# Optimization experiments

Measured on AMD Instinct MI355X. Metric: run time of the kernel, lower is better.

## Reference

```python
import jax, jax.numpy as jnp
import numpy as np

L, B, S, D, N, H = 4, 4, 1024, 1024, 64, 16   # layers, batch, seq, d_model, d_state, heads
DI = 2 * D      # d_inner (expand_factor=2)
DH = D // H     # head dim
DF = 4 * D      # ffn hidden
SCALE = 1.0 / np.sqrt(DH)


def setup_inputs() -> dict:
    key = jax.random.key(0)
    ks = jax.random.split(key, 12)
    w = lambda k, sh: jax.random.normal(k, sh, jnp.float32) * 0.02
    return {
        "x": jax.random.normal(ks[0], (B, S, D), jnp.float32),
        "A_log": jax.random.normal(ks[1], (L, N), jnp.float32),
        "Dp": jax.random.normal(ks[2], (L, D), jnp.float32),
        "W_in": w(ks[3], (L, 2 * DI, D)), "b_in": jnp.zeros((L, 2 * DI), jnp.float32),
        "W_xp": w(ks[4], (L, N, DI)), "b_xp": jnp.zeros((L, N), jnp.float32),
        "W_dt": w(ks[5], (L, D, DI)), "b_dt": jnp.zeros((L, D), jnp.float32),
        "W_out": w(ks[6], (L, D, DI)), "b_out": jnp.zeros((L, D), jnp.float32),
        "W_qkv": w(ks[7], (L, 3 * D, D)), "b_qkv": jnp.zeros((L, 3 * D), jnp.float32),
        "W_ao": w(ks[8], (L, D, D)), "b_ao": jnp.zeros((L, D), jnp.float32),
        "g1": jnp.ones((L, D), jnp.float32), "be1": jnp.zeros((L, D), jnp.float32),
        "g2": jnp.ones((L, D), jnp.float32), "be2": jnp.zeros((L, D), jnp.float32),
        "W_f1": w(ks[9], (L, DF, D)), "b_f1": jnp.zeros((L, DF), jnp.float32),
        "W_f2": w(ks[10], (L, D, DF)), "b_f2": jnp.zeros((L, D), jnp.float32),
    }


def _ln(x, g, b, eps=1e-5):
    mu = x.mean(-1, keepdims=True)
    var = ((x - mu) ** 2).mean(-1, keepdims=True)
    return (x - mu) * jax.lax.rsqrt(var + eps) * g + b


def _mamba(x, A_log, Dp, W_in, b_in, W_xp, b_xp, W_dt, b_dt, W_out, b_out):
    xr = jnp.einsum('bsd,od->bso', x, W_in) + b_in          # [b,s,2*DI]
    xi, res = jnp.split(xr, 2, axis=-1)
    xi = jax.nn.silu(xi)
    A = -jnp.exp(A_log)                                      # [N]
    delta = jax.nn.softplus(jnp.einsum('bsi,di->bsd', xi, W_dt) + b_dt)  # [b,s,D]
    m = delta.mean(-1)                                       # [b,s]
    A_disc = jnp.exp(A[None, None, :] * m[:, :, None])       # [b,s,N]
    u = jnp.einsum('bsi,ni->bsn', xi, W_xp) + b_xp           # [b,s,N]

    def step(state, inp):
        a_t, u_t = inp
        state = a_t * state + u_t                            # [b,N]
        return state, state.sum(-1)                          # carry, emit sum over d_state

    init = jnp.zeros((x.shape[0], A_log.shape[0]), x.dtype)
    _, ssum = jax.lax.scan(step, init, (A_disc.swapaxes(0, 1), u.swapaxes(0, 1)))
    ssum = ssum.swapaxes(0, 1)                               # [b,s]
    y = ssum[..., None] * xi                                 # [b,s,DI]
    y = y * jax.nn.silu(res)
    y = jnp.einsum('bsi,di->bsd', y, W_out) + b_out
    return y + x * Dp


def _attn(x, W_qkv, b_qkv, W_ao, b_ao):
    b, s, d = x.shape
    qkv = jnp.einsum('bsd,od->bso', x, W_qkv) + b_qkv        # [b,s,3d]
    qkv = qkv.reshape(b, s, 3, H, DH)
    q = jnp.moveaxis(qkv[:, :, 0], 2, 1)                     # [b,h,s,dh]
    k = jnp.moveaxis(qkv[:, :, 1], 2, 1)
    v = jnp.moveaxis(qkv[:, :, 2], 2, 1)
    scores = jnp.einsum('bhqd,bhkd->bhqk', q, k) * SCALE
    wts = jax.nn.softmax(scores, axis=-1)
    o = jnp.einsum('bhqk,bhkd->bhqd', wts, v)
    o = jnp.moveaxis(o, 1, 2).reshape(b, s, d)
    return jnp.einsum('bsd,od->bso', o, W_ao) + b_ao


def _forward(x, A_log, Dp, W_in, b_in, W_xp, b_xp, W_dt, b_dt, W_out, b_out,
             W_qkv, b_qkv, W_ao, b_ao, g1, be1, g2, be2, W_f1, b_f1, W_f2, b_f2):
    for l in range(L):
        m = _mamba(x, A_log[l], Dp[l], W_in[l], b_in[l], W_xp[l], b_xp[l],
                   W_dt[l], b_dt[l], W_out[l], b_out[l])
        x = _ln(x + m, g1[l], be1[l])
        a = _attn(x, W_qkv[l], b_qkv[l], W_ao[l], b_ao[l])
        x = _ln(x + a, g2[l], be2[l])
        h = jax.nn.gelu(jnp.einsum('bsd,fd->bsf', x, W_f1[l]) + b_f1[l], approximate=False)
        x = x + jnp.einsum('bsf,df->bsd', h, W_f2[l]) + b_f2[l]
    return x


def reference(x, A_log, Dp, W_in, b_in, W_xp, b_xp, W_dt, b_dt, W_out, b_out,
              W_qkv, b_qkv, W_ao, b_ao, g1, be1, g2, be2, W_f1, b_f1, W_f2, b_f2):
    return _forward(x, A_log, Dp, W_in, b_in, W_xp, b_xp, W_dt, b_dt, W_out, b_out,
                    W_qkv, b_qkv, W_ao, b_ao, g1, be1, g2, be2, W_f1, b_f1, W_f2, b_f2)
```

## Files before the change

kernel.cpp:

```cpp
#include <hip/hip_runtime.h>
#include <math.h>

typedef unsigned short ushort_t;
typedef unsigned int uint_t;
typedef __attribute__((ext_vector_type(8))) short short8;
typedef __attribute__((ext_vector_type(4))) float f32x4;

constexpr int Bb = 4, Ss = 1024, Dd = 1024, Nn = 64, Hh = 16;
constexpr int DIi = 2048, DFf = 4096;
constexpr int TOKENS = Bb * Ss;

constexpr size_t O_IN  = 0;
constexpr size_t O_DT  = 4194304;
constexpr size_t O_XP  = O_DT + 2097152;
constexpr size_t O_OUT = O_XP + 262144;
constexpr size_t O_QKV = O_OUT + 2097152;
constexpr size_t O_AO  = O_QKV + 3145728;
constexpr size_t O_F1  = O_AO + 1048576;
constexpr size_t O_F2  = O_F1 + 4194304;
constexpr size_t W_TOTAL = O_F2 + 4194304;
constexpr size_t W_QUADS = W_TOTAL / 4;

enum { EPI_SPLIT = 0, EPI_QKV, EPI_GELU, EPI_DTXP, EPI_DP, EPI_F32, EPI_RESID };

__device__ __forceinline__ float siluf(float x) { return x / (1.f + expf(-x)); }
__device__ __forceinline__ float softplusf(float x) { return fmaxf(x, 0.f) + log1pf(expf(-fabsf(x))); }
__device__ __forceinline__ float geluf(float x) { return 0.5f * x * (1.f + erff(x * 0.7071067811865476f)); }

__device__ __forceinline__ float bf2f(uint_t u) {
    union { uint_t i; float f; } v; v.i = u << 16; return v.f;
}
__device__ __forceinline__ ushort_t f2bf(float f) {
    union { float f; uint_t i; } v; v.f = f;
    return (ushort_t)((v.i + 0x7FFFu + ((v.i >> 16) & 1u)) >> 16);
}

__device__ __forceinline__ void gload_lds16(const ushort_t* g, ushort_t* l) {
    __builtin_amdgcn_global_load_lds(
        (const __attribute__((address_space(1))) unsigned int*)g,
        (__attribute__((address_space(3))) unsigned int*)l, 16, 0, 0);
}

__device__ __forceinline__ void wait_vm(int n) {
    if (n == 0)      asm volatile("s_waitcnt vmcnt(0)" ::: "memory");
    else if (n == 3) asm volatile("s_waitcnt vmcnt(3)" ::: "memory");
    else if (n == 4) asm volatile("s_waitcnt vmcnt(4)" ::: "memory");
    else if (n == 6) asm volatile("s_waitcnt vmcnt(6)" ::: "memory");
    else             asm volatile("s_waitcnt vmcnt(8)" ::: "memory");
}

template <int EPI>
__global__ __launch_bounds__(512, 2) void gemm_wide256(
    const ushort_t* __restrict__ A, const ushort_t* __restrict__ Bw,
    const float* __restrict__ bias, int M, int N, int K,
    ushort_t* __restrict__ ob0, ushort_t* __restrict__ ob1)
{
    __shared__ __attribute__((aligned(16))) ushort_t AB[65536];
    const int tid = threadIdx.x;
    const int lane = tid & 63, wid = tid >> 6;
    const int wr = wid >> 2, wc = wid & 3;
    const int l15 = lane & 15, lg = lane >> 4;

    int bx = blockIdx.x, by = blockIdx.y;
    const int gx = gridDim.x, gy = gridDim.y;
    if ((gy & 3) == 0 && (gx & 1) == 0) {
        const int s = by * gx + bx;
        const int xcd = s & 7, c = s >> 3;
        const int gyc = gy >> 2, gxc = gx >> 1;
        by = (xcd & 3) * gyc + (c % gyc);
        bx = (xcd >> 2) * gxc + (c / gyc);
    }
    const int m0 = by << 8, n0 = bx << 8;

    f32x4 acc[8][4];
#pragma unroll
    for (int i = 0; i < 8; ++i)
#pragma unroll
        for (int j = 0; j < 4; ++j) { acc[i][j][0]=0.f; acc[i][j][1]=0.f; acc[i][j][2]=0.f; acc[i][j][3]=0.f; }

    const int srow8 = lane >> 3;
    const int scc8  = (lane & 7) ^ srow8;
    const ushort_t* Ag = A + (size_t)(m0 + wid * 32 + srow8) * K + scc8 * 8;
    const ushort_t* Bg = Bw + (size_t)(n0 + wid * 32 + srow8) * K + scc8 * 8;

    auto STAGE = [&](int b_, int k0_) {
        ushort_t* d_ = AB + b_ * 32768;
#pragma unroll
        for (int i = 0; i < 4; ++i) {
            gload_lds16(Ag + (size_t)i * 8 * K + k0_, d_ + (wid * 32 + i * 8) * 64);
            gload_lds16(Bg + (size_t)i * 8 * K + k0_, d_ + 16384 + (wid * 32 + i * 8) * 64);
        }
    };

    const int NS = K >> 6;
    STAGE(0, 0);
    wait_vm(0);
    __builtin_amdgcn_s_barrier();
    int cur = 0;
    for (int s = 0; s < NS; ++s) {
        if (s + 1 < NS) STAGE(cur ^ 1, (s + 1) << 6);
        const ushort_t* As_ = AB + cur * 32768;
        const ushort_t* Bs_ = As_ + 16384;
#pragma unroll
        for (int kk = 0; kk < 2; ++kk) {
            short8 af[8], bfr[4];
#pragma unroll
            for (int mi = 0; mi < 8; ++mi) {
                const int row = wr * 128 + mi * 16 + l15;
                const int ch = (kk * 4 + lg) ^ (row & 7);
                af[mi] = *(const short8*)&As_[row * 64 + ch * 8];
            }
#pragma unroll
            for (int nj = 0; nj < 4; ++nj) {
                const int row = wc * 64 + nj * 16 + l15;
                const int ch = (kk * 4 + lg) ^ (row & 7);
                bfr[nj] = *(const short8*)&Bs_[row * 64 + ch * 8];
            }
#pragma unroll
            for (int mi = 0; mi < 8; ++mi)
#pragma unroll
                for (int nj = 0; nj < 4; ++nj)
                    acc[mi][nj] = __builtin_amdgcn_mfma_f32_16x16x32_bf16(
                        af[mi], bfr[nj], acc[mi][nj], 0, 0, 0);
        }
        if (s + 1 < NS) {
            wait_vm(0);
            __builtin_amdgcn_s_barrier();
        }
        cur ^= 1;
    }
    __syncthreads();

    const bool lo = (EPI != EPI_SPLIT) || (n0 < DIi);
#pragma unroll
    for (int nj = 0; nj < 4; ++nj) {
        const int coll = wc * 64 + nj * 16 + l15;
        const float bv = bias[n0 + coll];
#pragma unroll
        for (int mi = 0; mi < 8; ++mi)
#pragma unroll
            for (int r = 0; r < 4; ++r) {
                float v = acc[mi][nj][r] + bv;
                if (EPI == EPI_SPLIT) v = lo ? siluf(v) : v;
                else v = geluf(v);
                AB[(wr * 128 + mi * 16 + lg * 4 + r) * 256 + coll] = f2bf(v);
            }
    }
    __syncthreads();
    ushort_t* dst = (EPI == EPI_SPLIT) ? (lo ? ob0 : ob1) : ob0;
    const int Nd = (EPI == EPI_SPLIT) ? DIi : N;
    const int nb = (EPI == EPI_SPLIT && !lo) ? (n0 - DIi) : n0;
#pragma unroll
    for (int it = 0; it < 16; ++it) {
        const int c = it * 512 + tid;
        const int row = c >> 5, ch = c & 31;
        *(uint4*)&dst[(size_t)(m0 + row) * Nd + nb + ch * 8] =
            *(const uint4*)&AB[row * 256 + ch * 8];
    }
}

template <int EPI, int MT, int NBUF, int XBY>
__global__ __launch_bounds__(256) void gemm_mfma(
    const ushort_t* __restrict__ A, const ushort_t* __restrict__ Bw,
    const float* __restrict__ bias, int M, int N, int K,
    float* __restrict__ of0, float* __restrict__ of1,
    ushort_t* __restrict__ ob0, ushort_t* __restrict__ ob1,
    const float* __restrict__ e0, const float* __restrict__ e1)
{
    constexpr int BUFSZ = (MT == 128) ? 8192 : 6144;
    constexpr int DEPTH = NBUF - 1;
    constexpr int L     = (MT == 128) ? 4 : 3;
    constexpr int NJ    = (MT == 128) ? 4 : 2;
    constexpr int XBX   = 8 / XBY;
    __shared__ __attribute__((aligned(16))) ushort_t AB[NBUF * BUFSZ];

    const int tid = threadIdx.x;
    const int lane = tid & 63, wid = tid >> 6;
    const int wr = (MT == 128) ? (wid >> 1) : 0;
    const int wc = (MT == 128) ? (wid & 1) : wid;
    const int l15 = lane & 15, lg = lane >> 4;

    int bx = blockIdx.x, by = blockIdx.y;
    const int gx = gridDim.x, gy = gridDim.y;
    if ((gy % XBY) == 0 && (gx % XBX) == 0) {
        const int s = by * gx + bx;
        const int xcd = s & 7, c = s >> 3;
        const int gyc = gy / XBY, gxc = gx / XBX;
        by = (xcd % XBY) * gyc + (c % gyc);
        bx = (xcd / XBY) * gxc + (c / gyc);
    }
    const int m0 = by * MT, n0 = bx << 7;

    f32x4 acc[4][NJ];
#pragma unroll
    for (int i = 0; i < 4; ++i)
#pragma unroll
        for (int j = 0; j < NJ; ++j) { acc[i][j][0] = 0.f; acc[i][j][1] = 0.f; acc[i][j][2] = 0.f; acc[i][j][3] = 0.f; }

    const int srow4 = lane >> 2;
    const int scc4  = (lane & 3) ^ ((lane >> 3) & 3);
    const ushort_t* Ag = A + (size_t)(m0 + wid * 32 + srow4) * K + scc4 * 8;
    const ushort_t* Bg = Bw + (size_t)(n0 + wid * 32 + srow4) * K + scc4 * 8;
    const ushort_t* sb64[3];
    int do64[3];
    if (MT == 64) {
#pragma unroll
        for (int j = 0; j < 3; ++j) {
            const int i = wid * 3 + j;
            const bool isA = i < 4;
            const int rb = (isA ? i : i - 4) * 16;
            sb64[j] = (isA ? A + (size_t)(m0 + rb + srow4) * K
                           : Bw + (size_t)(n0 + rb + srow4) * K) + scc4 * 8;
            do64[j] = (isA ? 0 : 2048) + rb * 32;
        }
    }

    auto STAGE = [&](int b_, int k0_) {
        ushort_t* d_ = AB + b_ * BUFSZ;
        if constexpr (MT == 128) {
            gload_lds16(Ag + k0_,                  d_ + (wid * 32) * 32);
            gload_lds16(Ag + (size_t)16 * K + k0_, d_ + (wid * 32 + 16) * 32);
            gload_lds16(Bg + k0_,                  d_ + 4096 + (wid * 32) * 32);
            gload_lds16(Bg + (size_t)16 * K + k0_, d_ + 4096 + (wid * 32 + 16) * 32);
        } else {
#pragma unroll
            for (int j = 0; j < 3; ++j)
                gload_lds16(sb64[j] + k0_, d_ + do64[j]);
        }
    };

    const int NS = K >> 5;
#pragma unroll
    for (int p = 0; p < DEPTH; ++p) STAGE(p, p * 32);
    wait_vm((DEPTH - 1) * L);
    __builtin_amdgcn_s_barrier();

    const int chAB = (lg ^ ((l15 >> 1) & 3)) * 8;
    int bc = 0, bp = DEPTH;
    for (int s = 0; s < NS; ++s) {
        if (s + DEPTH < NS) STAGE(bp, (s + DEPTH) << 5);
        const ushort_t* As_ = AB + bc * BUFSZ;
        const ushort_t* Bs_ = As_ + ((MT == 128) ? 4096 : 2048);
        short8 af[4], bfr[NJ];
#pragma unroll
        for (int mi = 0; mi < 4; ++mi)
            af[mi] = *(const short8*)&As_[(wr * 64 + mi * 16 + l15) * 32 + chAB];
#pragma unroll
        for (int nj = 0; nj < NJ; ++nj)
            bfr[nj] = *(const short8*)&Bs_[(wc * (MT == 128 ? 64 : 32) + nj * 16 + l15) * 32 + chAB];
#pragma unroll
        for (int mi = 0; mi < 4; ++mi)
#pragma unroll
            for (int nj = 0; nj < NJ; ++nj)
                acc[mi][nj] = __builtin_amdgcn_mfma_f32_16x16x32_bf16(
                    af[mi], bfr[nj], acc[mi][nj], 0, 0, 0);
        if (s + 1 < NS) {
            const int rem = NS - 2 - s;
            wait_vm(((rem < DEPTH - 1) ? rem : DEPTH - 1) * L);
            __builtin_amdgcn_s_barrier();
        }
        bc = (bc + 1 == NBUF) ? 0 : bc + 1;
        bp = (bp + 1 == NBUF) ? 0 : bp + 1;
    }
    __syncthreads();

    if constexpr (MT == 128) {
        const bool lo = (EPI != EPI_SPLIT) || (n0 < DIi);
#pragma unroll
        for (int nj = 0; nj < 4; ++nj) {
            const int coll = wc * 64 + nj * 16 + l15;
            const float bv = bias[n0 + coll];
#pragma unroll
            for (int mi = 0; mi < 4; ++mi)
#pragma unroll
                for (int r = 0; r < 4; ++r) {
                    float v = acc[mi][nj][r] + bv;
                    if (EPI == EPI_SPLIT) v = lo ? siluf(v) : v;
                    else if (EPI == EPI_GELU) v = geluf(v);
                    AB[(wr * 64 + mi * 16 + lg * 4 + r) * 128 + coll] = f2bf(v);
                }
        }
        __syncthreads();
        if (EPI == EPI_QKV && n0 >= 2048) {
            const int bb = m0 >> 10, srow0 = m0 & 1023;
#pragma unroll
            for (int it = 0; it < 8; ++it) {
                const int task = it * 256 + tid;
                const int dim = task & 127;
                const int strip = task >> 7;
                uint_t w[4];
#pragma unroll
                for (int j = 0; j < 4; ++j) {
                    const int s2 = strip * 8 + 2 * j;
                    w[j] = (uint_t)AB[s2 * 128 + dim] | ((uint_t)AB[(s2 + 1) * 128 + dim] << 16);
                }
                const int vd = (n0 - 2048) + dim;
                *(uint4*)&ob1[((size_t)(bb * Hh + (vd >> 6)) * 64 + (vd & 63)) * Ss + srow0 + strip * 8] =
                    make_uint4(w[0], w[1], w[2], w[3]);
            }
        } else {
            ushort_t* dst = (EPI == EPI_SPLIT) ? (lo ? ob0 : ob1) : ob0;
            const int Nd = (EPI == EPI_SPLIT) ? DIi : N;
            const int nb = (EPI == EPI_SPLIT && !lo) ? (n0 - DIi) : n0;
#pragma unroll
            for (int i = 0; i < 8; ++i) {
                const int c = i * 256 + tid;
                const int row = c >> 4, ch = c & 15;
                *(uint4*)&dst[(size_t)(m0 + row) * Nd + nb + ch * 8] =
                    *(const uint4*)&AB[row * 128 + ch * 8];
            }
        }
    } else {
        float* Cf = (float*)AB;
#pragma unroll
        for (int nj = 0; nj < NJ; ++nj) {
            const int coll = wc * 32 + nj * 16 + l15;
            const float bv = bias[n0 + coll];
#pragma unroll
            for (int mi = 0; mi < 4; ++mi)
#pragma unroll
                for (int r = 0; r < 4; ++r)
                    Cf[(mi * 16 + lg * 4 + r) * 128 + coll] = acc[mi][nj][r] + bv;
        }
        __syncthreads();
#pragma unroll
        for (int i = 0; i < 8; ++i) {
            const int c = i * 256 + tid;
            const int row = c >> 5, ch = c & 31;
            const int grow = m0 + row;
            const int gcol = n0 + ch * 4;
            float4 v = *(const float4*)&Cf[row * 128 + ch * 4];
            if (EPI == EPI_DTXP) {
                if (n0 < Dd) {
                    float ps = softplusf(v.x) + softplusf(v.y) + softplusf(v.z) + softplusf(v.w);
#pragma unroll
                    for (int off = 1; off < 32; off <<= 1) ps += __shfl_xor(ps, off);
                    if ((lane & 31) == 0)
                        of0[(size_t)grow * 8 + (n0 >> 7)] = ps;
                } else {
                    *(float4*)&of1[(size_t)grow * 128 + (gcol - Dd)] = v;
                }
            } else if (EPI == EPI_DP) {
                const float4 e = *(const float4*)&e0[(size_t)grow * N + gcol];
                const float4 d = *(const float4*)&e1[gcol];
                v.x = fmaf(e.x, d.x, v.x); v.y = fmaf(e.y, d.y, v.y);
                v.z = fmaf(e.z, d.z, v.z); v.w = fmaf(e.w, d.w, v.w);
                *(float4*)&of0[(size_t)grow * N + gcol] = v;
            } else if (EPI == EPI_F32) {
                *(float4*)&of0[(size_t)grow * N + gcol] = v;
            } else {
                const float4 e = *(const float4*)&e0[(size_t)grow * N + gcol];
                v.x += e.x; v.y += e.y; v.z += e.z; v.w += e.w;
                *(float4*)&of0[(size_t)grow * N + gcol] = v;
                uint2 w;
                w.x = (uint_t)f2bf(v.x) | ((uint_t)f2bf(v.y) << 16);
                w.y = (uint_t)f2bf(v.z) | ((uint_t)f2bf(v.w) << 16);
                *(uint2*)&ob0[(size_t)grow * N + gcol] = w;
            }
        }
    }
}

__global__ __launch_bounds__(256) void convert_weights_kernel(
    const float* __restrict__ Win, const float* __restrict__ Wdt,
    const float* __restrict__ Wxp, const float* __restrict__ Wout,
    const float* __restrict__ Wqkv, const float* __restrict__ Wao,
    const float* __restrict__ Wf1, const float* __restrict__ Wf2,
    const float* __restrict__ bdt, const float* __restrict__ bxp,
    ushort_t* __restrict__ dst, float* __restrict__ bcat)
{
    size_t q = (size_t)blockIdx.x * blockDim.x + threadIdx.x;
    if (q < 288) {
#pragma unroll
        for (int j = 0; j < 4; ++j) {
            const int e = (int)q * 4 + j;
            bcat[e] = (e < Dd) ? bdt[e] : ((e < Dd + Nn) ? bxp[e - Dd] : 0.f);
        }
    }
    const size_t stride = (size_t)gridDim.x * blockDim.x;
    for (; q < W_QUADS; q += stride) {
        const size_t e = q * 4;
        float4 v;
        if (e < O_DT)       v = *(const float4*)&Win[e - O_IN];
        else if (e < O_XP)  v = *(const float4*)&Wdt[e - O_DT];
        else if (e < O_OUT) {
            const size_t li = e - O_XP;
            const int row = (int)(li >> 11), colq = (int)(li & 2047);
            v = (row < Nn) ? *(const float4*)&Wxp[(size_t)row * DIi + colq]
                           : make_float4(0.f, 0.f, 0.f, 0.f);
        }
        else if (e < O_QKV) v = *(const float4*)&Wout[e - O_OUT];
        else if (e < O_AO)  v = *(const float4*)&Wqkv[e - O_QKV];
        else if (e < O_F1)  v = *(const float4*)&Wao[e - O_AO];
        else if (e < O_F2)  v = *(const float4*)&Wf1[e - O_F1];
        else                v = *(const float4*)&Wf2[e - O_F2];
        uint2 w;
        w.x = (uint_t)f2bf(v.x) | ((uint_t)f2bf(v.y) << 16);
        w.y = (uint_t)f2bf(v.z) | ((uint_t)f2bf(v.w) << 16);
        *(uint2*)&dst[e] = w;
    }
}

__global__ __launch_bounds__(256) void cvt_f32_bf16_kernel(
    const float* __restrict__ in, ushort_t* __restrict__ out)
{
    const size_t i4 = (size_t)blockIdx.x * blockDim.x + threadIdx.x;
    const float4 v = *(const float4*)&in[i4 * 4];
    uint2 w;
    w.x = (uint_t)f2bf(v.x) | ((uint_t)f2bf(v.y) << 16);
    w.y = (uint_t)f2bf(v.z) | ((uint_t)f2bf(v.w) << 16);
    *(uint2*)&out[i4 * 4] = w;
}

__global__ __launch_bounds__(256) void ln_residual_kernel(
    float* __restrict__ xio, const float* __restrict__ addin,
    const float* __restrict__ g, const float* __restrict__ be,
    ushort_t* __restrict__ xb)
{
    __shared__ float red[8];
    const int tid = threadIdx.x;
    const size_t base = (size_t)blockIdx.x * Dd;
    const float4 xv = *(const float4*)&xio[base + tid * 4];
    const float4 av = *(const float4*)&addin[base + tid * 4];
    float v[4] = {xv.x + av.x, xv.y + av.y, xv.z + av.z, xv.w + av.w};
    float s = v[0] + v[1] + v[2] + v[3];
    float s2 = v[0] * v[0] + v[1] * v[1] + v[2] * v[2] + v[3] * v[3];
#pragma unroll
    for (int off = 32; off; off >>= 1) { s += __shfl_xor(s, off); s2 += __shfl_xor(s2, off); }
    if ((tid & 63) == 0) { red[tid >> 6] = s; red[4 + (tid >> 6)] = s2; }
    __syncthreads();
    const float mu = (red[0] + red[1] + red[2] + red[3]) * (1.f / (float)Dd);
    const float var = (red[4] + red[5] + red[6] + red[7]) * (1.f / (float)Dd) - mu * mu;
    const float rstd = rsqrtf(var + 1e-5f);
    const float4 gv = *(const float4*)&g[tid * 4];
    const float4 bv = *(const float4*)&be[tid * 4];
    float o[4];
    o[0] = (v[0] - mu) * rstd * gv.x + bv.x;
    o[1] = (v[1] - mu) * rstd * gv.y + bv.y;
    o[2] = (v[2] - mu) * rstd * gv.z + bv.z;
    o[3] = (v[3] - mu) * rstd * gv.w + bv.w;
    *(float4*)&xio[base + tid * 4] = make_float4(o[0], o[1], o[2], o[3]);
    uint2 w;
    w.x = (uint_t)f2bf(o[0]) | ((uint_t)f2bf(o[1]) << 16);
    w.y = (uint_t)f2bf(o[2]) | ((uint_t)f2bf(o[3]) << 16);
    *(uint2*)&xb[base + tid * 4] = w;
}

__global__ __launch_bounds__(1024) void scan_fused_kernel(
    const float* __restrict__ A_log_l, const float* __restrict__ part,
    const float* __restrict__ u, float* __restrict__ ssum)
{
    __shared__ float Ps[16][64];
    __shared__ float Sl[16][64];
    __shared__ float Cs[16][64];
    __shared__ float Ms[16][64];
    const int b = blockIdx.x;
    const int tid = threadIdx.x;
    const int n = tid & 63, c = tid >> 6;
    const int t0 = b * Ss + c * 64;
    const float Aval = -expf(A_log_l[n]);

    {
        const float* pp = part + (size_t)(t0 + n) * 8;
        float ps = 0.f;
#pragma unroll
        for (int j = 0; j < 8; ++j) ps += pp[j];
        Ms[c][n] = ps * (1.f / 1024.f);
    }
    __syncthreads();

    float S = 0.f, msum = 0.f;
#pragma unroll 8
    for (int t = 0; t < 64; ++t) {
        const float mt = Ms[c][t];
        msum += mt;
        S = fmaf(expf(Aval * mt), S, u[(size_t)(t0 + t) * 128 + n]);
    }
    Ps[c][n] = expf(Aval * msum);
    Sl[c][n] = S;
    __syncthreads();

    if (c == 0) {
        float carry = 0.f;
#pragma unroll
        for (int cc = 0; cc < 16; ++cc) {
            Cs[cc][n] = carry;
            carry = fmaf(Ps[cc][n], carry, Sl[cc][n]);
        }
    }
    __syncthreads();

    float st = Cs[c][n];
#pragma unroll 4
    for (int t = 0; t < 64; ++t) {
        st = fmaf(expf(Aval * Ms[c][t]), st, u[(size_t)(t0 + t) * 128 + n]);
        float r = st;
#pragma unroll
        for (int off = 32; off; off >>= 1) r += __shfl_xor(r, off);
        if (n == 0) ssum[t0 + t] = r;
    }
}

__global__ __launch_bounds__(256) void y_gate_kernel(
    ushort_t* __restrict__ xi, const ushort_t* __restrict__ res,
    const float* __restrict__ ssum)
{
    const size_t i8 = (size_t)blockIdx.x * blockDim.x + threadIdx.x;
    const int t = (int)(i8 >> 8);
    const float sv = ssum[t];
    uint4 xw = *(const uint4*)&xi[i8 * 8];
    const uint4 rw = *(const uint4*)&res[i8 * 8];
    const uint_t xs[4] = {xw.x, xw.y, xw.z, xw.w};
    const uint_t rs[4] = {rw.x, rw.y, rw.z, rw.w};
    uint_t os[4];
#pragma unroll
    for (int j = 0; j < 4; ++j) {
        const float x0 = bf2f(xs[j] & 0xffffu), x1 = bf2f(xs[j] >> 16);
        const float r0 = bf2f(rs[j] & 0xffffu), r1 = bf2f(rs[j] >> 16);
        os[j] = (uint_t)f2bf(sv * x0 * siluf(r0)) | ((uint_t)f2bf(sv * x1 * siluf(r1)) << 16);
    }
    *(uint4*)&xi[i8 * 8] = make_uint4(os[0], os[1], os[2], os[3]);
}

__global__ __launch_bounds__(256) void attn_mfma_kernel(
    const ushort_t* __restrict__ qkv, const ushort_t* __restrict__ vt,
    ushort_t* __restrict__ out)
{
    __shared__ ushort_t Ks[64 * 64];
    __shared__ ushort_t Vs[64 * 64];
    __shared__ __attribute__((aligned(16))) ushort_t Pb[4][2560];

    const int tid = threadIdx.x;
    const int lane = tid & 63, wid = tid >> 6;
    const int b = blockIdx.z, h = blockIdx.y;
    const int q0 = blockIdx.x * 128 + wid * 32;
    const int l15 = lane & 15, lg = lane >> 4;
    constexpr float CEXP = 0.125f * 1.44269504f;

    short8 qf[2][2];
#pragma unroll
    for (int mi = 0; mi < 2; ++mi)
#pragma unroll
        for (int kk = 0; kk < 2; ++kk)
            qf[mi][kk] = *(const short8*)&qkv[(size_t)(b * Ss + q0 + mi * 16 + l15) * 3072
                                              + h * 64 + kk * 32 + lg * 8];

    f32x4 oacc[2][4];
#pragma unroll
    for (int mi = 0; mi < 2; ++mi)
#pragma unroll
        for (int nj = 0; nj < 4; ++nj) { oacc[mi][nj][0]=0.f; oacc[mi][nj][1]=0.f; oacc[mi][nj][2]=0.f; oacc[mi][nj][3]=0.f; }
    float lrun[2][4];
#pragma unroll
    for (int mi = 0; mi < 2; ++mi)
#pragma unroll
        for (int r = 0; r < 4; ++r) lrun[mi][r] = 0.f;

    const int srow = lane >> 3;
    const int scc  = (lane & 7) ^ srow;
    const ushort_t* Kg = qkv + (size_t)(b * Ss + wid * 16 + srow) * 3072 + 1024 + h * 64 + scc * 8;
    const ushort_t* Vg = vt + (size_t)((b * Hh + h) * 64 + wid * 16 + srow) * Ss + scc * 8;

    for (int kt = 0; kt < Ss / 64; ++kt) {
#pragma unroll
        for (int j = 0; j < 2; ++j) {
            gload_lds16(Kg + (size_t)(kt * 64 + j * 8) * 3072, Ks + (wid * 16 + j * 8) * 64);
            gload_lds16(Vg + (size_t)j * 8 * Ss + kt * 64,     Vs + (wid * 16 + j * 8) * 64);
        }
        __syncthreads();

        f32x4 sacc[2][4];
#pragma unroll
        for (int mi = 0; mi < 2; ++mi)
#pragma unroll
            for (int nj = 0; nj < 4; ++nj) { sacc[mi][nj][0]=0.f; sacc[mi][nj][1]=0.f; sacc[mi][nj][2]=0.f; sacc[mi][nj][3]=0.f; }
#pragma unroll
        for (int kk = 0; kk < 2; ++kk) {
            short8 kf[4];
#pragma unroll
            for (int nj = 0; nj < 4; ++nj) {
                const int row = nj * 16 + l15;
                const int ch = (kk * 4 + lg) ^ (row & 7);
                kf[nj] = *(const short8*)&Ks[row * 64 + ch * 8];
            }
#pragma unroll
            for (int mi = 0; mi < 2; ++mi)
#pragma unroll
                for (int nj = 0; nj < 4; ++nj)
                    sacc[mi][nj] = __builtin_amdgcn_mfma_f32_16x16x32_bf16(
                        qf[mi][kk], kf[nj], sacc[mi][nj], 0, 0, 0);
        }

#pragma unroll
        for (int mi = 0; mi < 2; ++mi)
#pragma unroll
            for (int nj = 0; nj < 4; ++nj) {
                const int bi = mi * 2 + (nj >> 1);
                const int chsw = ((nj & 1) * 2 + (l15 >> 3)) ^ lg;
#pragma unroll
                for (int r = 0; r < 4; ++r) {
                    const float p = exp2f(sacc[mi][nj][r] * CEXP);
                    lrun[mi][r] += p;
                    const int q15 = lg * 4 + r;
                    Pb[wid][bi * 640 + q15 * 40 + chsw * 8 + (lane & 7)] = f2bf(p);
                }
            }

#pragma unroll
        for (int kk = 0; kk < 2; ++kk) {
            short8 pa[2], vb[4];
#pragma unroll
            for (int mi = 0; mi < 2; ++mi) {
                const int chsw = lg ^ (l15 >> 2);
                pa[mi] = *(const short8*)&Pb[wid][(mi * 2 + kk) * 640 + l15 * 40 + chsw * 8];
            }
#pragma unroll
            for (int nj = 0; nj < 4; ++nj) {
                const int row = nj * 16 + l15;
                const int ch = (kk * 4 + lg) ^ (row & 7);
                vb[nj] = *(const short8*)&Vs[row * 64 + ch * 8];
            }
#pragma unroll
            for (int mi = 0; mi < 2; ++mi)
#pragma unroll
                for (int nj = 0; nj < 4; ++nj)
                    oacc[mi][nj] = __builtin_amdgcn_mfma_f32_16x16x32_bf16(
                        pa[mi], vb[nj], oacc[mi][nj], 0, 0, 0);
        }
        __syncthreads();
    }

#pragma unroll
    for (int mi = 0; mi < 2; ++mi)
#pragma unroll
        for (int r = 0; r < 4; ++r) {
            float s = lrun[mi][r];
#pragma unroll
            for (int off = 1; off < 16; off <<= 1) s += __shfl_xor(s, off);
            lrun[mi][r] = 1.f / s;
        }
#pragma unroll
    for (int mi = 0; mi < 2; ++mi)
#pragma unroll
        for (int r = 0; r < 4; ++r) {
            const int q = q0 + mi * 16 + lg * 4 + r;
            const float inv = lrun[mi][r];
#pragma unroll
            for (int nj = 0; nj < 4; ++nj)
                out[(size_t)(b * Ss + q) * Dd + h * 64 + nj * 16 + l15] =
                    f2bf(oacc[mi][nj][r] * inv);
        }
}

extern "C" void kernel_launch(void* const* d_in, const int* in_sizes, int n_in,
                              void* d_out, int out_size, void* d_ws, size_t ws_size,
                              hipStream_t stream)
{
    const float* x_in  = (const float*)d_in[0];
    const float* A_log = (const float*)d_in[1];
    const float* Dp    = (const float*)d_in[2];
    const float* W_in  = (const float*)d_in[3];
    const float* b_in  = (const float*)d_in[4];
    const float* W_xp  = (const float*)d_in[5];
    const float* b_xp  = (const float*)d_in[6];
    const float* W_dt  = (const float*)d_in[7];
    const float* b_dt  = (const float*)d_in[8];
    const float* W_out = (const float*)d_in[9];
    const float* b_out = (const float*)d_in[10];
    const float* W_qkv = (const float*)d_in[11];
    const float* b_qkv = (const float*)d_in[12];
    const float* W_ao  = (const float*)d_in[13];
    const float* b_ao  = (const float*)d_in[14];
    const float* g1    = (const float*)d_in[15];
    const float* be1   = (const float*)d_in[16];
    const float* g2    = (const float*)d_in[17];
    const float* be2   = (const float*)d_in[18];
    const float* W_f1  = (const float*)d_in[19];
    const float* b_f1  = (const float*)d_in[20];
    const float* W_f2  = (const float*)d_in[21];
    const float* b_f2  = (const float*)d_in[22];

    float* xf      = (float*)d_ws;
    float* a3      = xf + 4194304;
    float* ub      = a3 + 4194304;
    float* sb      = ub + 524288;
    float* part    = sb + 4096;
    float* bcat    = part + 32768;
    ushort_t* xb    = (ushort_t*)(bcat + 1152);
    ushort_t* xi_b  = xb + 4194304;
    ushort_t* res_b = xi_b + 8388608;
    ushort_t* qh_b  = res_b + 8388608;
    ushort_t* ao_b  = qh_b + 16777216;
    ushort_t* Wb    = ao_b + 4194304;
    ushort_t* vt_b  = Wb + W_TOTAL;

    hipMemcpyAsync(xf, x_in, (size_t)TOKENS * Dd * sizeof(float),
                   hipMemcpyDeviceToDevice, stream);
    cvt_f32_bf16_kernel<<<dim3(4096), dim3(256), 0, stream>>>(x_in, xb);

    const dim3 blk(256), blk512(512);

    for (int l = 0; l < 4; ++l) {
        convert_weights_kernel<<<dim3(2048), blk, 0, stream>>>(
            W_in + (size_t)l * 4194304, W_dt + (size_t)l * 2097152,
            W_xp + (size_t)l * 131072,  W_out + (size_t)l * 2097152,
            W_qkv + (size_t)l * 3145728, W_ao + (size_t)l * 1048576,
            W_f1 + (size_t)l * 4194304, W_f2 + (size_t)l * 4194304,
            b_dt + (size_t)l * 1024, b_xp + (size_t)l * Nn, Wb, bcat);

        gemm_wide256<EPI_SPLIT><<<dim3(16, 16), blk512, 0, stream>>>(
            xb, Wb + O_IN, b_in + (size_t)l * 4096, TOKENS, 4096, 1024,
            xi_b, res_b);
        gemm_mfma<EPI_DTXP, 64, 4, 8><<<dim3(9, 64), blk, 0, stream>>>(
            xi_b, Wb + O_DT, bcat, TOKENS, 1152, 2048,
            part, ub, nullptr, nullptr, nullptr, nullptr);
        scan_fused_kernel<<<dim3(Bb), dim3(1024), 0, stream>>>(
            A_log + (size_t)l * Nn, part, ub, sb);
        y_gate_kernel<<<dim3(4096), blk, 0, stream>>>(xi_b, res_b, sb);
        gemm_mfma<EPI_DP, 64, 4, 8><<<dim3(8, 64), blk, 0, stream>>>(
            xi_b, Wb + O_OUT, b_out + (size_t)l * 1024, TOKENS, 1024, 2048,
            a3, nullptr, nullptr, nullptr, xf, Dp + (size_t)l * 1024);
        ln_residual_kernel<<<dim3(TOKENS), blk, 0, stream>>>(
            xf, a3, g1 + (size_t)l * 1024, be1 + (size_t)l * 1024, xb);
        gemm_mfma<EPI_QKV, 128, 3, 4><<<dim3(24, 32), blk, 0, stream>>>(
            xb, Wb + O_QKV, b_qkv + (size_t)l * 3072, TOKENS, 3072, 1024,
            nullptr, nullptr, qh_b, vt_b, nullptr, nullptr);
        attn_mfma_kernel<<<dim3(8, Hh, Bb), blk, 0, stream>>>(qh_b, vt_b, ao_b);
        gemm_mfma<EPI_F32, 64, 4, 8><<<dim3(8, 64), blk, 0, stream>>>(
            ao_b, Wb + O_AO, b_ao + (size_t)l * 1024, TOKENS, 1024, 1024,
            a3, nullptr, nullptr, nullptr, nullptr, nullptr);
        ln_residual_kernel<<<dim3(TOKENS), blk, 0, stream>>>(
            xf, a3, g2 + (size_t)l * 1024, be2 + (size_t)l * 1024, xb);
        gemm_wide256<EPI_GELU><<<dim3(16, 16), blk512, 0, stream>>>(
            xb, Wb + O_F1, b_f1 + (size_t)l * 4096, TOKENS, 4096, 1024,
            qh_b, nullptr);
        gemm_mfma<EPI_RESID, 64, 4, 8><<<dim3(8, 64), blk, 0, stream>>>(
            qh_b, Wb + O_F2, b_f2 + (size_t)l * 1024, TOKENS, 1024, 4096,
            xf, nullptr, xb, nullptr, xf, nullptr);
    }

    hipMemcpyAsync(d_out, xf, (size_t)TOKENS * Dd * sizeof(float),
                   hipMemcpyDeviceToDevice, stream);
    (void)in_sizes; (void)n_in; (void)out_size; (void)ws_size;
}
```

Baseline: 1.728 ms.

## Double-buffer K/V tiles in attention kernel with async prefetch and setprio

Doubles the LDS K and V tiles so the next 64-key tile is loaded asynchronously while MFMA work runs on the current one. A vmcnt wait and raw s_barrier replace the __syncthreads that previously stalled on every tile load. s_setprio is raised around the MFMA phases to favour matrix issue. This adds LDS use (16KB more per block), which may reduce occupancy, and depends on the vmcnt count correctly tracking the outstanding loads.

```diff
diff --git a/kernel.cpp b/kernel.cpp
--- a/kernel.cpp
+++ b/kernel.cpp
@@ -526,8 +526,8 @@
     const ushort_t* __restrict__ qkv, const ushort_t* __restrict__ vt,
     ushort_t* __restrict__ out)
 {
-    __shared__ ushort_t Ks[64 * 64];
-    __shared__ ushort_t Vs[64 * 64];
+    __shared__ ushort_t Ks[2][64 * 64];
+    __shared__ ushort_t Vs[2][64 * 64];
     __shared__ __attribute__((aligned(16))) ushort_t Pb[4][2560];
 
     const int tid = threadIdx.x;
@@ -561,19 +561,28 @@
     const ushort_t* Kg = qkv + (size_t)(b * Ss + wid * 16 + srow) * 3072 + 1024 + h * 64 + scc * 8;
     const ushort_t* Vg = vt + (size_t)((b * Hh + h) * 64 + wid * 16 + srow) * Ss + scc * 8;
 
-    for (int kt = 0; kt < Ss / 64; ++kt) {
+    auto STAGE_KV = [&](int buf, int kt) {
 #pragma unroll
         for (int j = 0; j < 2; ++j) {
-            gload_lds16(Kg + (size_t)(kt * 64 + j * 8) * 3072, Ks + (wid * 16 + j * 8) * 64);
-            gload_lds16(Vg + (size_t)j * 8 * Ss + kt * 64,     Vs + (wid * 16 + j * 8) * 64);
-        }
-        __syncthreads();
+            gload_lds16(Kg + (size_t)(kt * 64 + j * 8) * 3072, Ks[buf] + (wid * 16 + j * 8) * 64);
+            gload_lds16(Vg + (size_t)j * 8 * Ss + kt * 64,     Vs[buf] + (wid * 16 + j * 8) * 64);
+        }
+    };
+
+    constexpr int NT = Ss / 64;
+    STAGE_KV(0, 0);
+    int cur = 0;
+    for (int kt = 0; kt < NT; ++kt) {
+        if (kt + 1 < NT) STAGE_KV(cur ^ 1, kt + 1);
+        wait_vm((kt + 1 < NT) ? 4 : 0);
+        __builtin_amdgcn_s_barrier();
 
         f32x4 sacc[2][4];
 #pragma unroll
         for (int mi = 0; mi < 2; ++mi)
 #pragma unroll
             for (int nj = 0; nj < 4; ++nj) { sacc[mi][nj][0]=0.f; sacc[mi][nj][1]=0.f; sacc[mi][nj][2]=0.f; sacc[mi][nj][3]=0.f; }
+        __builtin_amdgcn_s_setprio(1);
 #pragma unroll
         for (int kk = 0; kk < 2; ++kk) {
             short8 kf[4];
@@ -581,7 +590,7 @@
             for (int nj = 0; nj < 4; ++nj) {
                 const int row = nj * 16 + l15;
                 const int ch = (kk * 4 + lg) ^ (row & 7);
-                kf[nj] = *(const short8*)&Ks[row * 64 + ch * 8];
+                kf[nj] = *(const short8*)&Ks[cur][row * 64 + ch * 8];
             }
 #pragma unroll
             for (int mi = 0; mi < 2; ++mi)
@@ -590,6 +599,7 @@
                     sacc[mi][nj] = __builtin_amdgcn_mfma_f32_16x16x32_bf16(
                         qf[mi][kk], kf[nj], sacc[mi][nj], 0, 0, 0);
         }
+        __builtin_amdgcn_s_setprio(0);
 
 #pragma unroll
         for (int mi = 0; mi < 2; ++mi)
@@ -606,6 +616,7 @@
                 }
             }
 
+        __builtin_amdgcn_s_setprio(1);
 #pragma unroll
         for (int kk = 0; kk < 2; ++kk) {
             short8 pa[2], vb[4];
@@ -618,7 +629,7 @@
             for (int nj = 0; nj < 4; ++nj) {
                 const int row = nj * 16 + l15;
                 const int ch = (kk * 4 + lg) ^ (row & 7);
-                vb[nj] = *(const short8*)&Vs[row * 64 + ch * 8];
+                vb[nj] = *(const short8*)&Vs[cur][row * 64 + ch * 8];
             }
 #pragma unroll
             for (int mi = 0; mi < 2; ++mi)
@@ -627,7 +638,11 @@
                     oacc[mi][nj] = __builtin_amdgcn_mfma_f32_16x16x32_bf16(
                         pa[mi], vb[nj], oacc[mi][nj], 0, 0, 0);
         }
-        __syncthreads();
+        __builtin_amdgcn_s_setprio(0);
+
+        asm volatile("s_waitcnt lgkmcnt(0)" ::: "memory");
+        __builtin_amdgcn_s_barrier();
+        cur ^= 1;
     }
 
 #pragma unroll
```

Measured after the change: 1.723 ms. Within noise of the previous version (-0.3%).
